# Performance work log

Measured on AMD Instinct MI355X. Metric: run time of the kernel, lower is better.

Reference implementation:

```python
import jax, jax.numpy as jnp
import numpy as np

N, T, S = 8192, 512, 32
D = 256          # d_model (h_states feature dim)
H = 256          # query_mlp_hidden_dim
R = 256          # operator rank
RFF = 64
DT = 16
L = 2            # num_query_mlp_layers
NHEAD = 4
HD = H // NHEAD
EPS = 1e-5


def _ln(x, g, b):
    m = jnp.mean(x, axis=-1, keepdims=True)
    v = jnp.mean((x - m) ** 2, axis=-1, keepdims=True)
    return (x - m) * jax.lax.rsqrt(v + EPS) * g + b


def _lin(x, w, b):  # torch Linear: w is [out, in]
    return x @ w.T + b


def rff_encode(x, B):
    p = x @ B
    return jnp.concatenate([jnp.cos(p), jnp.sin(p)], axis=-1)


def setup_inputs() -> dict:
    key = jax.random.key(0)
    ks = iter(jax.random.split(key, 64))
    rn = lambda shape, s=0.05: jax.random.normal(next(ks), shape, jnp.float32) * s
    inp = {}
    inp['xy'] = jax.random.uniform(next(ks), (N, 2), jnp.float32) * 2 * np.pi
    inp['t_q'] = jax.random.uniform(next(ks), (N,), jnp.float32)
    inp['c'] = jax.random.randint(next(ks), (N,), 0, 3)
    inp['h_states'] = rn((T, S, D), 1.0)
    inp['sensor_time'] = jnp.sort(jax.random.uniform(next(ks), (T,), jnp.float32))
    inp['B'] = rn((2, RFF), 1.0)
    q_in = 2 * RFF + DT + 8
    inp['time_w'] = rn((DT, 1)); inp['time_b'] = jnp.zeros((DT,))
    inp['comp_emb'] = rn((3, 8), 0.1)
    inp['trunk_in_w'] = rn((H, q_in)); inp['trunk_in_b'] = jnp.zeros((H,))
    inp['blk_ln_g'] = jnp.ones((L, H)); inp['blk_ln_b'] = jnp.zeros((L, H))
    inp['blk_fc1_w'] = rn((L, H, H)); inp['blk_fc1_b'] = jnp.zeros((L, H))
    inp['blk_fc2_w'] = rn((L, H, H)); inp['blk_fc2_b'] = jnp.zeros((L, H))
    inp['btp_w'] = rn((H, D)); inp['btp_b'] = jnp.zeros((H,))
    inp['bn_g'] = jnp.ones((H,)); inp['bn_b'] = jnp.zeros((H,))
    inp['attn_in_w'] = rn((3 * H, H)); inp['attn_in_b'] = jnp.zeros((3 * H,))
    inp['attn_out_w'] = rn((H, H)); inp['attn_out_b'] = jnp.zeros((H,))
    inp['bc_ln_g'] = jnp.ones((H,)); inp['bc_ln_b'] = jnp.zeros((H,))
    inp['bc_w1'] = rn((H, H)); inp['bc_b1'] = jnp.zeros((H,))
    inp['bc_w2'] = rn((H, H)); inp['bc_b2'] = jnp.zeros((H,))
    inp['trunk_out_w'] = rn((3 * R, H)); inp['trunk_out_b'] = jnp.zeros((3 * R,))
    inp['bproj_w'] = rn((3 * R, H)); inp['bproj_b'] = jnp.zeros((3 * R,))
    inp['log_temp'] = jnp.asarray(np.log(1.0 / np.sqrt(R)), jnp.float32)
    inp['comp_scale'] = jnp.ones((3,)); inp['comp_bias'] = jnp.zeros((3,))
    return inp


def reference(xy, t_q, c, h_states, sensor_time, B, time_w, time_b, comp_emb,
              trunk_in_w, trunk_in_b, blk_ln_g, blk_ln_b, blk_fc1_w, blk_fc1_b,
              blk_fc2_w, blk_fc2_b, btp_w, btp_b, bn_g, bn_b,
              attn_in_w, attn_in_b, attn_out_w, attn_out_b,
              bc_ln_g, bc_ln_b, bc_w1, bc_b1, bc_w2, bc_b2,
              trunk_out_w, trunk_out_b, bproj_w, bproj_b,
              log_temp, comp_scale, comp_bias):
    n = xy.shape[0]
    # time-indexed gather of CfC states
    idx = jnp.searchsorted(sensor_time, t_q, side='right') - 1
    idx = jnp.clip(idx, 0, h_states.shape[0] - 1)
    h_br = h_states[idx]                                   # [N,S,D]
    dt = jnp.maximum(t_q - sensor_time[idx], 0.0)          # [N]
    # trunk path
    rff = rff_encode(xy, B)                                # [N,2*RFF]
    time_e = _lin(dt[:, None], time_w, time_b)             # [N,DT]
    emb_c = comp_emb[c]                                    # [N,8]
    feat = jax.nn.silu(_lin(jnp.concatenate([rff, time_e, emb_c], -1), trunk_in_w, trunk_in_b))
    for i in range(blk_fc1_w.shape[0]):
        y = _ln(feat, blk_ln_g[i], blk_ln_b[i])
        y = jax.nn.silu(_lin(y, blk_fc1_w[i], blk_fc1_b[i]))
        feat = feat + _lin(y, blk_fc2_w[i], blk_fc2_b[i])
    trunk_basis = _lin(feat, trunk_out_w, trunk_out_b).reshape(n, 3, -1)
    # branch path: single-query cross attention over sensor tokens
    tokens = _lin(h_br, btp_w, btp_b)                      # [N,S,H]
    q_in = _ln(feat, bn_g, bn_b)                           # [N,H]
    wq, wk, wv = jnp.split(attn_in_w, 3, axis=0)
    bq, bk, bv = jnp.split(attn_in_b, 3, axis=0)
    q = (q_in @ wq.T + bq).reshape(n, NHEAD, HD)           # [N,h,d]
    k = (tokens @ wk.T + bk).reshape(n, S, NHEAD, HD)
    v = (tokens @ wv.T + bv).reshape(n, S, NHEAD, HD)
    scores = jnp.einsum('nhd,nshd->nhs', q, k) / jnp.sqrt(jnp.asarray(HD, q.dtype))
    attn = jax.nn.softmax(scores, axis=-1)
    ctx = jnp.einsum('nhs,nshd->nhd', attn, v).reshape(n, -1)
    ctx = ctx @ attn_out_w.T + attn_out_b                  # [N,H]
    y = _ln(ctx, bc_ln_g, bc_ln_b)
    y = jax.nn.silu(_lin(y, bc_w1, bc_b1))
    ctx = ctx + _lin(y, bc_w2, bc_b2)
    branch_basis = _lin(ctx, bproj_w, bproj_b).reshape(n, 3, -1)
    # per-component select + rank-contraction fusion
    ar = jnp.arange(n)
    trunk_sel = trunk_basis[ar, c]                         # [N,R]
    branch_sel = branch_basis[ar, c]
    temp = jnp.exp(log_temp).astype(trunk_sel.dtype)
    out = jnp.sum(trunk_sel * branch_sel, axis=1, keepdims=True) * temp
    return out * comp_scale[c][:, None] + comp_bias[c][:, None]
```

## Files before the change

kernel.cpp:

```cpp
#include <hip/hip_runtime.h>
#include <cstdint>
#include <cstddef>

typedef unsigned short u16;
typedef __attribute__((ext_vector_type(8))) short s16x8;
typedef __attribute__((ext_vector_type(4))) float f32x4;

#define NQ   8192
#define TT   512
#define STOK 32
#define LDF  260

__device__ __forceinline__ float b2f(u16 u) {
    return __uint_as_float(((uint32_t)u) << 16);
}
__device__ __forceinline__ u16 f2b(float f) {
    uint32_t x = __float_as_uint(f);
    uint32_t r = (x + 0x7FFFu + ((x >> 16) & 1u)) >> 16;
    return (u16)r;
}
__device__ __forceinline__ float silu_f(float x) { return x / (1.f + expf(-x)); }

__global__ __launch_bounds__(256) void const_kernel(float v, float* __restrict__ out) {
    int i = blockIdx.x * 256 + threadIdx.x;
    if (i < NQ) out[i] = v;
}

__global__ __launch_bounds__(256) void zero_kernel(int* __restrict__ cnt) {
    int i = blockIdx.x * 256 + threadIdx.x;
    if (i < 512) cnt[i] = 0;
}

__global__ __launch_bounds__(256) void feat32_kernel(
    const float* __restrict__ xy, const float* __restrict__ t_q,
    const int* __restrict__ c, const float* __restrict__ st,
    const float* __restrict__ B, const float* __restrict__ tw,
    const float* __restrict__ tb, const float* __restrict__ ce,
    float* __restrict__ FIN, int* __restrict__ IDX) {
    int n = blockIdx.x, t = threadIdx.x;
    float tq = t_q[n];
    int lo = 0, hi = TT;
    while (lo < hi) {
        int mid = (lo + hi) >> 1;
        if (st[mid] <= tq) lo = mid + 1; else hi = mid;
    }
    int idx = lo - 1;
    if (idx < 0) idx = 0;
    float dt = tq - st[idx];
    if (dt < 0.f) dt = 0.f;
    if (t == 0) IDX[n] = idx;
    float x = xy[2 * n], y = xy[2 * n + 1];
    size_t base = (size_t)n * 160;
    if (t < 64) { float p = x * B[t] + y * B[64 + t]; FIN[base + t] = cosf(p); }
    else if (t < 128) { int j = t - 64; float p = x * B[j] + y * B[64 + j]; FIN[base + t] = sinf(p); }
    else if (t < 144) { int j = t - 128; FIN[base + t] = dt * tw[j] + tb[j]; }
    else if (t < 152) { int j = t - 144; FIN[base + t] = ce[c[n] * 8 + j]; }
    else if (t < 160) { FIN[base + t] = 0.f; }
}

__global__ __launch_bounds__(256) void pack_split(
    const float* __restrict__ f1w, const float* __restrict__ f2w,
    const float* __restrict__ aiw, const float* __restrict__ aow,
    const float* __restrict__ w1, const float* __restrict__ w2,
    const float* __restrict__ tiw,
    u16* __restrict__ PH, u16* __restrict__ PL) {
    int i = blockIdx.x * 256 + threadIdx.x;
    if (i >= 565248) return;
    float v;
    size_t pos;
    if (i < 524288) {
        int m = i >> 16, j = i & 65535;
        int col = j >> 8, k = j & 255;
        const float* src;
        switch (m) {
            case 0: src = f1w; break;
            case 1: src = f1w + 65536; break;
            case 2: src = f2w; break;
            case 3: src = f2w + 65536; break;
            case 4: src = aiw; break;
            case 5: src = aow; break;
            case 6: src = w1; break;
            default: src = w2; break;
        }
        v = src[j];
        int ct = col >> 4, m16 = col & 15, k0 = k >> 5, quad = (k >> 3) & 3, jj = k & 7;
        pos = (size_t)m * 65536 + (size_t)(((ct * 8 + k0) * 64 + quad * 16 + m16) * 8 + jj);
    } else {
        int j = i - 524288;
        int col = j / 160, k = j % 160;
        v = (k < 152) ? tiw[col * 152 + k] : 0.f;
        int ct = col >> 4, m16 = col & 15, k0 = k >> 5, quad = (k >> 3) & 3, jj = k & 7;
        pos = 524288 + (size_t)(((ct * 5 + k0) * 64 + quad * 16 + m16) * 8 + jj);
    }
    u16 h = f2b(v);
    PH[pos] = h;
    PL[pos] = f2b(v - b2f(h));
}

__global__ __launch_bounds__(256) void combine_kv32(
    const float* __restrict__ aiw, const float* __restrict__ aib,
    const float* __restrict__ btw, const float* __restrict__ btb,
    u16* __restrict__ WKVb, float* __restrict__ bkv) {
    int kv = blockIdx.x >> 8, m = blockIdx.x & 255;
    int d = threadIdx.x;
    __shared__ float wrow[256];
    wrow[d] = aiw[(size_t)(kv + 1) * 65536 + (size_t)m * 256 + d];
    __syncthreads();
    float acc = 0.f;
#pragma unroll 8
    for (int o = 0; o < 256; o++) acc += wrow[o] * btw[(size_t)o * 256 + d];
    WKVb[(size_t)kv * 65536 + (size_t)m * 256 + d] = f2b(acc);
    float pb = wrow[d] * btb[d];
#pragma unroll
    for (int mm = 32; mm >= 1; mm >>= 1) pb += __shfl_xor(pb, mm);
    __shared__ float red[4];
    if ((d & 63) == 0) red[d >> 6] = pb;
    __syncthreads();
    if (d == 0)
        bkv[kv * 256 + m] = red[0] + red[1] + red[2] + red[3] + aib[(kv + 1) * 256 + m];
}

__global__ __launch_bounds__(256) void mcat_kernel(const float* __restrict__ tow,
                                                   const float* __restrict__ bpw,
                                                   u16* __restrict__ MCATb) {
    const int cc = blockIdx.z;
    const int t0 = blockIdx.x * 16, k0 = blockIdx.y * 16;
    const int lt = threadIdx.x & 15, lj = threadIdx.x >> 4;
    const int ot = threadIdx.x & 15, ok = threadIdx.x >> 4;
    __shared__ float As[16][17], Bs[16][17];
    float acc = 0.f;
    for (int j0 = 0; j0 < 256; j0 += 16) {
        As[lj][lt] = tow[((size_t)cc * 256 + j0 + lj) * 256 + t0 + lt];
        Bs[lj][lt] = bpw[((size_t)cc * 256 + j0 + lj) * 256 + k0 + lt];
        __syncthreads();
#pragma unroll
        for (int jj = 0; jj < 16; jj++) acc += As[jj][ot] * Bs[jj][ok];
        __syncthreads();
    }
    MCATb[((size_t)cc * 256 + t0 + ot) * 256 + k0 + ok] = f2b(acc);
}

__global__ __launch_bounds__(256) void uvs_kernel(
    const float* __restrict__ tow, const float* __restrict__ tob,
    const float* __restrict__ bpw, const float* __restrict__ bpb,
    float* __restrict__ U, float* __restrict__ V, float* __restrict__ S) {
    const int cc = blockIdx.x, t = threadIdx.x;
    float v = 0.f, u = 0.f;
    for (int r = 0; r < 256; r++) {
        v += tow[((size_t)cc * 256 + r) * 256 + t] * bpb[cc * 256 + r];
        u += bpw[((size_t)cc * 256 + r) * 256 + t] * tob[cc * 256 + r];
    }
    V[cc * 256 + t] = v;
    U[cc * 256 + t] = u;
    float sp = tob[cc * 256 + t] * bpb[cc * 256 + t];
#pragma unroll
    for (int m = 32; m >= 1; m >>= 1) sp += __shfl_xor(sp, m);
    __shared__ float red[4];
    if ((t & 63) == 0) red[t >> 6] = sp;
    __syncthreads();
    if (t == 0) S[cc] = red[0] + red[1] + red[2] + red[3];
}

__global__ __launch_bounds__(256) void hist_kernel(const int* __restrict__ IDX,
                                                   int* __restrict__ cnt) {
    int n = blockIdx.x * 256 + threadIdx.x;
    if (n < NQ) atomicAdd(&cnt[IDX[n]], 1);
}
__global__ __launch_bounds__(512) void scan_kernel(const int* __restrict__ cnt,
                                                   int* __restrict__ base,
                                                   int* __restrict__ cur) {
    __shared__ int s[TT];
    int t = threadIdx.x;
    int v = cnt[t];
    s[t] = v;
    __syncthreads();
    for (int off = 1; off < TT; off <<= 1) {
        int add = (t >= off) ? s[t - off] : 0;
        __syncthreads();
        s[t] += add;
        __syncthreads();
    }
    base[t] = s[t] - v;
    cur[t] = s[t] - v;
}
__global__ __launch_bounds__(256) void scat_kernel(const int* __restrict__ IDX,
                                                   int* __restrict__ cur,
                                                   int* __restrict__ perm) {
    int n = blockIdx.x * 256 + threadIdx.x;
    if (n < NQ) {
        int pos = atomicAdd(&cur[IDX[n]], 1);
        perm[pos] = n;
    }
}

template <int ST16, int SEL>
__global__ __launch_bounds__(256) void mgemm_b(
    const float* __restrict__ A, const u16* __restrict__ Wb,
    const float* __restrict__ bias, const int* __restrict__ csel,
    void* __restrict__ Cv, int ldc) {
    __shared__ u16 As[64 * 40];
    __shared__ u16 Ws[64 * 40];
    const int t = threadIdx.x;
    const size_t rb = (size_t)blockIdx.x * 64;
    const size_t cb = (size_t)blockIdx.y * 64;
    const int wave = t >> 6, lane = t & 63;
    const int m16 = lane & 15, quad = lane >> 4;
    const int sr = t >> 2, sk = (t & 3) * 8;
    const float* Ap = A + (rb + sr) * 256 + sk;
    const u16* Wp = Wb + (cb + sr) * 256 + sk;

    f32x4 acc[4] = {};
    for (int k0 = 0; k0 < 256; k0 += 32) {
        float4 a0 = *(const float4*)(Ap + k0);
        float4 a1 = *(const float4*)(Ap + k0 + 4);
        u16 ta[8] = {f2b(a0.x), f2b(a0.y), f2b(a0.z), f2b(a0.w),
                     f2b(a1.x), f2b(a1.y), f2b(a1.z), f2b(a1.w)};
        *(uint4*)&As[sr * 40 + sk] = *(const uint4*)ta;
        *(uint4*)&Ws[sr * 40 + sk] = *(const uint4*)(Wp + k0);
        __syncthreads();
        s16x8 af = *(const s16x8*)&As[(wave * 16 + m16) * 40 + quad * 8];
#pragma unroll
        for (int ct = 0; ct < 4; ct++) {
            s16x8 bf = *(const s16x8*)&Ws[(ct * 16 + m16) * 40 + quad * 8];
            acc[ct] = __builtin_amdgcn_mfma_f32_16x16x32_bf16(af, bf, acc[ct], 0, 0, 0);
        }
        __syncthreads();
    }
#pragma unroll
    for (int ct = 0; ct < 4; ct++) {
        size_t col = cb + ct * 16 + m16;
        float bb = bias ? bias[col] : 0.f;
#pragma unroll
        for (int r = 0; r < 4; r++) {
            size_t row = rb + wave * 16 + quad * 4 + r;
            float x = acc[ct][r] + bb;
            if (SEL) {
                int comp = (int)(col >> 8);
                if (csel[row] == comp)
                    ((float*)Cv)[row * 256 + (col & 255)] = x;
            } else if (ST16) {
                ((u16*)Cv)[row * (size_t)ldc + col] = f2b(x);
            } else {
                ((float*)Cv)[row * (size_t)ldc + col] = x;
            }
        }
    }
}

template <int NK0>
struct WF { s16x8 h[NK0], l[NK0]; };

template <int NK0>
__device__ __forceinline__ void wload(const u16* __restrict__ PH,
                                      const u16* __restrict__ PL, size_t mb,
                                      int wave, int lane, WF<NK0>& w) {
#pragma unroll
    for (int k0 = 0; k0 < NK0; k0++) {
        const size_t wo = mb + ((size_t)(wave * NK0 + k0) * 64 + lane) * 8;
        w.h[k0] = *(const s16x8*)&PH[wo];
        w.l[k0] = *(const s16x8*)&PL[wo];
    }
}

template <int NK0>
__device__ __forceinline__ void cgemm_c(const WF<NK0>& w,
                                        const u16* Ch, const u16* Cl,
                                        int lane, f32x4 (&acc)[2]) {
    acc[0] = (f32x4){0.f, 0.f, 0.f, 0.f};
    acc[1] = (f32x4){0.f, 0.f, 0.f, 0.f};
#pragma unroll
    for (int k0 = 0; k0 < NK0; k0++) {
        s16x8 a0h = *(const s16x8*)&Ch[(k0 * 64 + lane) * 8];
        s16x8 a0l = *(const s16x8*)&Cl[(k0 * 64 + lane) * 8];
        s16x8 a1h = *(const s16x8*)&Ch[((8 + k0) * 64 + lane) * 8];
        s16x8 a1l = *(const s16x8*)&Cl[((8 + k0) * 64 + lane) * 8];
        acc[0] = __builtin_amdgcn_mfma_f32_16x16x32_bf16(a0h, w.h[k0], acc[0], 0, 0, 0);
        acc[0] = __builtin_amdgcn_mfma_f32_16x16x32_bf16(a0l, w.h[k0], acc[0], 0, 0, 0);
        acc[0] = __builtin_amdgcn_mfma_f32_16x16x32_bf16(a0h, w.l[k0], acc[0], 0, 0, 0);
        acc[1] = __builtin_amdgcn_mfma_f32_16x16x32_bf16(a1h, w.h[k0], acc[1], 0, 0, 0);
        acc[1] = __builtin_amdgcn_mfma_f32_16x16x32_bf16(a1l, w.h[k0], acc[1], 0, 0, 0);
        acc[1] = __builtin_amdgcn_mfma_f32_16x16x32_bf16(a1h, w.l[k0], acc[1], 0, 0, 0);
    }
}

__device__ __forceinline__ void ln_split(const float* __restrict__ Fv,
                                         u16* __restrict__ Ch, u16* __restrict__ Cl,
                                         const float* __restrict__ g,
                                         const float* __restrict__ b,
                                         float* __restrict__ mean_s,
                                         float* __restrict__ rstd_s, int t) {
    {
        const int row = t >> 5, q = t & 31;
        const float* fr = Fv + row * LDF;
        float4 v0 = *(const float4*)&fr[q * 4];
        float4 v1 = *(const float4*)&fr[q * 4 + 128];
        float s1 = v0.x + v0.y + v0.z + v0.w + v1.x + v1.y + v1.z + v1.w;
        float s2 = v0.x * v0.x + v0.y * v0.y + v0.z * v0.z + v0.w * v0.w +
                   v1.x * v1.x + v1.y * v1.y + v1.z * v1.z + v1.w * v1.w;
#pragma unroll
        for (int m = 16; m >= 1; m >>= 1) {
            s1 += __shfl_xor(s1, m);
            s2 += __shfl_xor(s2, m);
        }
        if (q == 0) {
            float mean = s1 * (1.f / 256.f);
            mean_s[row] = mean;
            rstd_s[row] = rsqrtf(s2 * (1.f / 256.f) - mean * mean + 1e-5f);
        }
    }
    __syncthreads();
    {
        const int rw = t & 31, qc = t >> 5;
        const float* fr = Fv + rw * LDF + qc * 8;
        float4 v0 = *(const float4*)fr;
        float4 v1 = *(const float4*)(fr + 4);
        const float mean = mean_s[rw], rstd = rstd_s[rw];
        float4 g0 = *(const float4*)&g[qc * 8], g1 = *(const float4*)&g[qc * 8 + 4];
        float4 b0 = *(const float4*)&b[qc * 8], b1 = *(const float4*)&b[qc * 8 + 4];
        float va[8] = {v0.x, v0.y, v0.z, v0.w, v1.x, v1.y, v1.z, v1.w};
        float ga[8] = {g0.x, g0.y, g0.z, g0.w, g1.x, g1.y, g1.z, g1.w};
        float ba[8] = {b0.x, b0.y, b0.z, b0.w, b1.x, b1.y, b1.z, b1.w};
        u16 hv[8], lv[8];
#pragma unroll
        for (int j = 0; j < 8; j++) {
            float x = (va[j] - mean) * rstd * ga[j] + ba[j];
            hv[j] = f2b(x);
            lv[j] = f2b(x - b2f(hv[j]));
        }
        const int c = qc * 8;
        const int off = (((rw >> 4) * 8 + (c >> 5)) * 64 +
                         (((c >> 3) & 3) * 16 + (rw & 15))) * 8;
        *(uint4*)&Ch[off] = *(const uint4*)hv;
        *(uint4*)&Cl[off] = *(const uint4*)lv;
    }
}

__global__ __launch_bounds__(1024) void chain1_kernel(
    const float* __restrict__ FIN, const u16* __restrict__ PH,
    const u16* __restrict__ PL, const float* __restrict__ tib,
    const float* __restrict__ lng, const float* __restrict__ lnb,
    const float* __restrict__ f1b, const float* __restrict__ f2bv,
    const float* __restrict__ bng, const float* __restrict__ bnb,
    const float* __restrict__ aib,
    float* __restrict__ Qb, float* __restrict__ Fg) {
    __shared__ u16 Ch[8192], Cl[8192];
    __shared__ float Fv[32 * LDF];
    __shared__ float mean_s[32], rstd_s[32];
    const int t = threadIdx.x;
    const int wave = t >> 6, lane = t & 63;
    const int m16 = lane & 15, quad = lane >> 4;
    const size_t rb = (size_t)blockIdx.x * 32;
    const int col = wave * 16 + m16;
    f32x4 acc[2];

    {
        const int row = t >> 5, q = t & 31;
        if (q < 20) {
            const float* p = FIN + (rb + row) * 160 + q * 8;
            float4 v0 = *(const float4*)p, v1 = *(const float4*)(p + 4);
            float va[8] = {v0.x, v0.y, v0.z, v0.w, v1.x, v1.y, v1.z, v1.w};
            u16 hv[8], lv[8];
#pragma unroll
            for (int j = 0; j < 8; j++) { hv[j] = f2b(va[j]); lv[j] = f2b(va[j] - b2f(hv[j])); }
            const int c = q * 8;
            const int off = (((row >> 4) * 8 + (c >> 5)) * 64 +
                             (((c >> 3) & 3) * 16 + (row & 15))) * 8;
            *(uint4*)&Ch[off] = *(const uint4*)hv;
            *(uint4*)&Cl[off] = *(const uint4*)lv;
        }
    }

    {
        WF<5> w;
        wload<5>(PH, PL, 524288, wave, lane, w);
        __syncthreads();
        cgemm_c<5>(w, Ch, Cl, lane, acc);
    }
    {
        const float bb = tib[col];
#pragma unroll
        for (int rt = 0; rt < 2; rt++)
#pragma unroll
            for (int r = 0; r < 4; r++)
                Fv[(rt * 16 + quad * 4 + r) * LDF + col] = silu_f(acc[rt][r] + bb);
    }
    __syncthreads();

#pragma unroll
    for (int L = 0; L < 2; L++) {
        ln_split(Fv, Ch, Cl, lng + L * 256, lnb + L * 256, mean_s, rstd_s, t);
        {
            WF<8> w;
            wload<8>(PH, PL, (size_t)L * 65536, wave, lane, w);
            __syncthreads();
            cgemm_c<8>(w, Ch, Cl, lane, acc);
        }
        __syncthreads();
        {
            const float bb = f1b[L * 256 + col];
            const int k0c = col >> 5, qc4 = (col >> 3) & 3, jc = col & 7;
#pragma unroll
            for (int rt = 0; rt < 2; rt++)
#pragma unroll
                for (int r = 0; r < 4; r++) {
                    const int row = rt * 16 + quad * 4 + r;
                    float x = silu_f(acc[rt][r] + bb);
                    const int off = ((rt * 8 + k0c) * 64 + (qc4 * 16 + (row & 15))) * 8 + jc;
                    u16 h = f2b(x);
                    Ch[off] = h;
                    Cl[off] = f2b(x - b2f(h));
                }
        }
        {
            WF<8> w;
            wload<8>(PH, PL, 131072 + (size_t)L * 65536, wave, lane, w);
            __syncthreads();
            cgemm_c<8>(w, Ch, Cl, lane, acc);
        }
        {
            const float bb = f2bv[L * 256 + col];
#pragma unroll
            for (int rt = 0; rt < 2; rt++)
#pragma unroll
                for (int r = 0; r < 4; r++) {
                    const int row = rt * 16 + quad * 4 + r;
                    Fv[row * LDF + col] += acc[rt][r] + bb;
                }
        }
        __syncthreads();
    }

    {
        const int row = t >> 5, q = t & 31;
        const float* fr = Fv + row * LDF + q * 8;
        float4 v0 = *(const float4*)fr, v1 = *(const float4*)(fr + 4);
        float* dst = Fg + (rb + row) * 256 + q * 8;
        *(float4*)dst = v0;
        *(float4*)(dst + 4) = v1;
    }
    ln_split(Fv, Ch, Cl, bng, bnb, mean_s, rstd_s, t);

    {
        WF<8> w;
        wload<8>(PH, PL, 262144, wave, lane, w);
        __syncthreads();
        cgemm_c<8>(w, Ch, Cl, lane, acc);
    }
    {
        const float bb = aib[col];
#pragma unroll
        for (int rt = 0; rt < 2; rt++)
#pragma unroll
            for (int r = 0; r < 4; r++) {
                const int row = rt * 16 + quad * 4 + r;
                Qb[(rb + row) * 256 + col] = acc[rt][r] + bb;
            }
    }
}

__global__ __launch_bounds__(1024) void chain2_kernel(
    const float* __restrict__ CTX, const u16* __restrict__ PH,
    const u16* __restrict__ PL, const float* __restrict__ aob,
    const float* __restrict__ clg, const float* __restrict__ clb,
    const float* __restrict__ b1, const float* __restrict__ b2v,
    float* __restrict__ C2g) {
    __shared__ u16 Ch[8192], Cl[8192];
    __shared__ float Fv[32 * LDF];
    __shared__ float mean_s[32], rstd_s[32];
    const int t = threadIdx.x;
    const int wave = t >> 6, lane = t & 63;
    const int m16 = lane & 15, quad = lane >> 4;
    const size_t rb = (size_t)blockIdx.x * 32;
    const int col = wave * 16 + m16;
    f32x4 acc[2];

    {
        const int row = t >> 5, q = t & 31;
        const float* p = CTX + (rb + row) * 256 + q * 8;
        float4 v0 = *(const float4*)p, v1 = *(const float4*)(p + 4);
        float va[8] = {v0.x, v0.y, v0.z, v0.w, v1.x, v1.y, v1.z, v1.w};
        u16 hv[8], lv[8];
#pragma unroll
        for (int j = 0; j < 8; j++) { hv[j] = f2b(va[j]); lv[j] = f2b(va[j] - b2f(hv[j])); }
        const int c = q * 8;
        const int off = (((row >> 4) * 8 + (c >> 5)) * 64 +
                         (((c >> 3) & 3) * 16 + (row & 15))) * 8;
        *(uint4*)&Ch[off] = *(const uint4*)hv;
        *(uint4*)&Cl[off] = *(const uint4*)lv;
    }

    {
        WF<8> w;
        wload<8>(PH, PL, 327680, wave, lane, w);
        __syncthreads();
        cgemm_c<8>(w, Ch, Cl, lane, acc);
    }
    {
        const float bb = aob[col];
#pragma unroll
        for (int rt = 0; rt < 2; rt++)
#pragma unroll
            for (int r = 0; r < 4; r++)
                Fv[(rt * 16 + quad * 4 + r) * LDF + col] = acc[rt][r] + bb;
    }
    __syncthreads();

    ln_split(Fv, Ch, Cl, clg, clb, mean_s, rstd_s, t);
    {
        WF<8> w;
        wload<8>(PH, PL, 393216, wave, lane, w);
        __syncthreads();
        cgemm_c<8>(w, Ch, Cl, lane, acc);
    }
    __syncthreads();
    {
        const float bb = b1[col];
        const int k0c = col >> 5, qc4 = (col >> 3) & 3, jc = col & 7;
#pragma unroll
        for (int rt = 0; rt < 2; rt++)
#pragma unroll
            for (int r = 0; r < 4; r++) {
                const int row = rt * 16 + quad * 4 + r;
                float x = silu_f(acc[rt][r] + bb);
                const int off = ((rt * 8 + k0c) * 64 + (qc4 * 16 + (row & 15))) * 8 + jc;
                u16 h = f2b(x);
                Ch[off] = h;
                Cl[off] = f2b(x - b2f(h));
            }
    }
    {
        WF<8> w;
        wload<8>(PH, PL, 458752, wave, lane, w);
        __syncthreads();
        cgemm_c<8>(w, Ch, Cl, lane, acc);
    }
    {
        const float bb = b2v[col];
#pragma unroll
        for (int rt = 0; rt < 2; rt++)
#pragma unroll
            for (int r = 0; r < 4; r++) {
                const int row = rt * 16 + quad * 4 + r;
                C2g[(rb + row) * 256 + col] = acc[rt][r] + bb + Fv[row * LDF + col];
            }
    }
}

__global__ __launch_bounds__(256) void attn4_kernel(
    float* __restrict__ QC, const u16* __restrict__ KV,
    const int* __restrict__ idx, const int* __restrict__ perm) {
    __shared__ u16 vsh[STOK * 264];
    __shared__ float qsh[256], attw[4][STOK];
    const int n = perm[blockIdx.x];
    const int t = threadIdx.x;
    qsh[t] = QC[(size_t)n * 256 + t];
    int ii = idx[n];
    ii = ii < 0 ? 0 : (ii > TT - 1 ? TT - 1 : ii);
    const u16* kvb = KV + (size_t)ii * STOK * 512;
#pragma unroll
    for (int i = t; i < 1024; i += 256) {
        int s = i >> 5, dq = (i & 31) * 8;
        *(uint4*)&vsh[s * 264 + dq] = *(const uint4*)&kvb[(size_t)s * 512 + 256 + dq];
    }
    __syncthreads();
    if (t < 128) {
        int h = t >> 5, s = t & 31;
        const u16* kp = kvb + (size_t)s * 512 + h * 64;
        uint4 kv[8];
#pragma unroll
        for (int dq = 0; dq < 8; dq++) kv[dq] = *(const uint4*)(kp + dq * 8);
        float p0 = 0.f, p1 = 0.f;
#pragma unroll
        for (int dq = 0; dq < 8; dq++) {
            const u16* ks = (const u16*)&kv[dq];
            float a0 = 0.f;
#pragma unroll
            for (int j = 0; j < 8; j++) a0 += qsh[h * 64 + dq * 8 + j] * b2f(ks[j]);
            if (dq & 1) p1 += a0; else p0 += a0;
        }
        float sc = (p0 + p1) * 0.125f;
        float mx = sc;
#pragma unroll
        for (int m = 16; m >= 1; m >>= 1) mx = fmaxf(mx, __shfl_xor(mx, m));
        float e = expf(sc - mx);
        float sum = e;
#pragma unroll
        for (int m = 16; m >= 1; m >>= 1) sum += __shfl_xor(sum, m);
        attw[h][s] = e / sum;
    }
    __syncthreads();
    {
        int h = t >> 6;
        float a = 0.f;
#pragma unroll 8
        for (int s = 0; s < STOK; s++) a += attw[h][s] * b2f(vsh[s * 264 + t]);
        QC[(size_t)n * 256 + t] = a;
    }
}

__global__ __launch_bounds__(256) void dot_kernel(
    const float* __restrict__ F, const float* __restrict__ H,
    const float* __restrict__ C2, const int* __restrict__ c,
    const float* __restrict__ U, const float* __restrict__ V,
    const float* __restrict__ S, const float* __restrict__ lt,
    const float* __restrict__ cs, const float* __restrict__ cbv,
    float* __restrict__ out) {
    const int n = blockIdx.x * 4 + (threadIdx.x >> 6);
    const int lane = threadIdx.x & 63;
    const int cc = c[n];
    float4 f4 = *(const float4*)&F[(size_t)n * 256 + lane * 4];
    float4 h4 = *(const float4*)&H[(size_t)n * 256 + lane * 4];
    float4 g4 = *(const float4*)&C2[(size_t)n * 256 + lane * 4];
    float4 v4 = *(const float4*)&V[cc * 256 + lane * 4];
    float4 u4 = *(const float4*)&U[cc * 256 + lane * 4];
    float a = f4.x * (h4.x + v4.x) + f4.y * (h4.y + v4.y) +
              f4.z * (h4.z + v4.z) + f4.w * (h4.w + v4.w) +
              u4.x * g4.x + u4.y * g4.y + u4.z * g4.z + u4.w * g4.w;
#pragma unroll
    for (int m = 32; m >= 1; m >>= 1) a += __shfl_xor(a, m);
    if (lane == 0)
        out[n] = (a + S[cc]) * expf(lt[0]) * cs[cc] + cbv[cc];
}

extern "C" void kernel_launch(void* const* d_in, const int* in_sizes, int n_in,
                              void* d_out, int out_size, void* d_ws, size_t ws_size,
                              hipStream_t stream) {
    float* out = (float*)d_out;
    const dim3 blk(256);

    static const int EXPECT[38] = {
        16384, 8192, 8192, 4194304, 512, 128, 16, 16, 24,
        38912, 256, 512, 512, 131072, 512, 131072, 512,
        65536, 256, 256, 256, 196608, 768, 65536, 256,
        256, 256, 65536, 256, 65536, 256, 196608, 768,
        196608, 768, 1, 3, 3};
    if (n_in != 38) { const_kernel<<<NQ / 256, blk, 0, stream>>>(99.0e6f, out); return; }
    for (int i = 0; i < 38; i++)
        if (in_sizes[i] != EXPECT[i]) {
            const_kernel<<<NQ / 256, blk, 0, stream>>>((100.0f + i) * 1.0e6f, out);
            return;
        }

    const float* xy  = (const float*)d_in[0];
    const float* tq  = (const float*)d_in[1];
    const int*   c   = (const int*)d_in[2];
    const float* hs  = (const float*)d_in[3];
    const float* st  = (const float*)d_in[4];
    const float* Bm  = (const float*)d_in[5];
    const float* tw  = (const float*)d_in[6];
    const float* tbv = (const float*)d_in[7];
    const float* ce  = (const float*)d_in[8];
    const float* tiw = (const float*)d_in[9];
    const float* tib = (const float*)d_in[10];
    const float* lng = (const float*)d_in[11];
    const float* lnb = (const float*)d_in[12];
    const float* f1w = (const float*)d_in[13];
    const float* f1b = (const float*)d_in[14];
    const float* f2w = (const float*)d_in[15];
    const float* f2b_ = (const float*)d_in[16];
    const float* btw = (const float*)d_in[17];
    const float* btb = (const float*)d_in[18];
    const float* bng = (const float*)d_in[19];
    const float* bnb = (const float*)d_in[20];
    const float* aiw = (const float*)d_in[21];
    const float* aib = (const float*)d_in[22];
    const float* aow = (const float*)d_in[23];
    const float* aob = (const float*)d_in[24];
    const float* clg = (const float*)d_in[25];
    const float* clb = (const float*)d_in[26];
    const float* w1  = (const float*)d_in[27];
    const float* b1  = (const float*)d_in[28];
    const float* w2  = (const float*)d_in[29];
    const float* b2  = (const float*)d_in[30];
    const float* tow = (const float*)d_in[31];
    const float* tob = (const float*)d_in[32];
    const float* bpw = (const float*)d_in[33];
    const float* bpb = (const float*)d_in[34];
    const float* lt  = (const float*)d_in[35];
    const float* cs  = (const float*)d_in[36];
    const float* cbv = (const float*)d_in[37];

    char* ws = (char*)d_ws;
    const size_t MB = 1 << 20;
    if (ws_size < 44 * MB) {
        const_kernel<<<NQ / 256, blk, 0, stream>>>(8.0e6f, out);
        return;
    }

    u16*   KV   = (u16*)(ws + 0 * MB);
    char*  S_A  = ws + 16 * MB;
    char*  S_B  = ws + 24 * MB;
    char*  S_C  = ws + 32 * MB;
    char*  misc = ws + 40 * MB;
    float* FIN  = (float*)S_A;
    float* H    = (float*)S_A;
    float* F    = (float*)S_B;
    float* Qb   = (float*)S_C;
    float* C2   = (float*)S_C;
    int*   IDX  = (int*)(misc + 0);
    float* bkv  = (float*)(misc + 32 * 1024);
    float* Ubuf = (float*)(misc + 36 * 1024);
    float* Vbuf = (float*)(misc + 40 * 1024);
    float* Sbuf = (float*)(misc + 44 * 1024);
    int*   CNT  = (int*)(misc + 48 * 1024);
    int*   BASE = (int*)(misc + 52 * 1024);
    int*   CUR  = (int*)(misc + 56 * 1024);
    int*   PERM = (int*)(misc + 60 * 1024);
    u16*   WKVb = (u16*)(misc + 92 * 1024);
    u16*   MCATb= (u16*)(misc + 348 * 1024);
    u16*   PH   = (u16*)(misc + 732 * 1024);
    u16*   PL   = (u16*)(misc + 1836 * 1024);

    const dim3 gKV(TT * STOK / 64, 8);
    const dim3 gSEL(NQ / 64, 12);

    zero_kernel<<<2, blk, 0, stream>>>(CNT);
    pack_split<<<2208, blk, 0, stream>>>(f1w, f2w, aiw, aow, w1, w2, tiw, PH, PL);
    combine_kv32<<<512, blk, 0, stream>>>(aiw, aib, btw, btb, WKVb, bkv);
    mcat_kernel<<<dim3(16, 16, 3), blk, 0, stream>>>(tow, bpw, MCATb);
    uvs_kernel<<<3, blk, 0, stream>>>(tow, tob, bpw, bpb, Ubuf, Vbuf, Sbuf);
    feat32_kernel<<<NQ, blk, 0, stream>>>(xy, tq, c, st, Bm, tw, tbv, ce, FIN, IDX);

    hist_kernel<<<NQ / 256, blk, 0, stream>>>(IDX, CNT);
    scan_kernel<<<1, dim3(512), 0, stream>>>(CNT, BASE, CUR);
    scat_kernel<<<NQ / 256, blk, 0, stream>>>(IDX, CUR, PERM);

    mgemm_b<1, 0><<<gKV, blk, 0, stream>>>(hs, WKVb, bkv, nullptr, KV, 512);

    chain1_kernel<<<NQ / 32, dim3(1024), 0, stream>>>(FIN, PH, PL, tib, lng, lnb,
                                                      f1b, f2b_, bng, bnb, aib, Qb, F);
    attn4_kernel<<<NQ, blk, 0, stream>>>(Qb, KV, IDX, PERM);
    chain2_kernel<<<NQ / 32, dim3(1024), 0, stream>>>(Qb, PH, PL, aob, clg, clb,
                                                      b1, b2, C2);
    mgemm_b<0, 1><<<gSEL, blk, 0, stream>>>(C2, MCATb, nullptr, c, H, 256);
    dot_kernel<<<NQ / 4, blk, 0, stream>>>(F, H, C2, c, Ubuf, Vbuf, Sbuf, lt, cs, cbv, out);
}
```

Measured before the change: 322.1 us.

## Fuse weight-prep and feature kernels into one block-dispatched launch

Merges pack_split, combine_kv32, mcat_kernel, uvs_kernel and feat32_kernel into a single prep_all kernel that picks its role by block index ranges. The uvs work is also split from 3 blocks into 24 blocks that combine partial sums with atomicAdd, and zero_kernel now zeroes U and V first. The aim is to remove several launch gaps and the serial tail of the long 3-block uvs kernel. In exchange, all roles share one register/LDS footprint, and float atomics make the order of the U/V summation nondeterministic.

Measured after the change: 286.2 us. 11.2% less time.

```diff
diff --git a/kernel.cpp b/kernel.cpp
--- a/kernel.cpp
+++ b/kernel.cpp
@@ -11,6 +11,12 @@
 #define STOK 32
 #define LDF  260
 
+#define PB_PACK 2208
+#define PB_COMB (PB_PACK + 512)
+#define PB_MCAT (PB_COMB + 768)
+#define PB_UVS  (PB_MCAT + 24)
+#define PB_TOT  (PB_UVS + NQ)
+
 __device__ __forceinline__ float b2f(u16 u) {
     return __uint_as_float(((uint32_t)u) << 16);
 }
@@ -26,139 +32,144 @@
     if (i < NQ) out[i] = v;
 }
 
-__global__ __launch_bounds__(256) void zero_kernel(int* __restrict__ cnt) {
+__global__ __launch_bounds__(256) void zero_kernel(int* __restrict__ cnt,
+                                                   float* __restrict__ U,
+                                                   float* __restrict__ V) {
     int i = blockIdx.x * 256 + threadIdx.x;
     if (i < 512) cnt[i] = 0;
-}
-
-__global__ __launch_bounds__(256) void feat32_kernel(
+    else if (i < 1280) U[i - 512] = 0.f;
+    else if (i < 2048) V[i - 1280] = 0.f;
+}
+
+__global__ __launch_bounds__(256) void prep_all(
+    const float* __restrict__ f1w, const float* __restrict__ f2w,
+    const float* __restrict__ aiw, const float* __restrict__ aow,
+    const float* __restrict__ w1, const float* __restrict__ w2,
+    const float* __restrict__ tiw,
+    u16* __restrict__ PH, u16* __restrict__ PL,
+    const float* __restrict__ aib, const float* __restrict__ btw,
+    const float* __restrict__ btb, u16* __restrict__ WKVb,
+    float* __restrict__ bkv,
+    const float* __restrict__ tow, const float* __restrict__ bpw,
+    u16* __restrict__ MCATb,
+    const float* __restrict__ tob, const float* __restrict__ bpb,
+    float* __restrict__ U, float* __restrict__ V, float* __restrict__ S,
     const float* __restrict__ xy, const float* __restrict__ t_q,
     const int* __restrict__ c, const float* __restrict__ st,
     const float* __restrict__ B, const float* __restrict__ tw,
     const float* __restrict__ tb, const float* __restrict__ ce,
     float* __restrict__ FIN, int* __restrict__ IDX) {
-    int n = blockIdx.x, t = threadIdx.x;
-    float tq = t_q[n];
-    int lo = 0, hi = TT;
-    while (lo < hi) {
-        int mid = (lo + hi) >> 1;
-        if (st[mid] <= tq) lo = mid + 1; else hi = mid;
-    }
-    int idx = lo - 1;
-    if (idx < 0) idx = 0;
-    float dt = tq - st[idx];
-    if (dt < 0.f) dt = 0.f;
-    if (t == 0) IDX[n] = idx;
-    float x = xy[2 * n], y = xy[2 * n + 1];
-    size_t base = (size_t)n * 160;
-    if (t < 64) { float p = x * B[t] + y * B[64 + t]; FIN[base + t] = cosf(p); }
-    else if (t < 128) { int j = t - 64; float p = x * B[j] + y * B[64 + j]; FIN[base + t] = sinf(p); }
-    else if (t < 144) { int j = t - 128; FIN[base + t] = dt * tw[j] + tb[j]; }
-    else if (t < 152) { int j = t - 144; FIN[base + t] = ce[c[n] * 8 + j]; }
-    else if (t < 160) { FIN[base + t] = 0.f; }
-}
-
-__global__ __launch_bounds__(256) void pack_split(
-    const float* __restrict__ f1w, const float* __restrict__ f2w,
-    const float* __restrict__ aiw, const float* __restrict__ aow,
-    const float* __restrict__ w1, const float* __restrict__ w2,
-    const float* __restrict__ tiw,
-    u16* __restrict__ PH, u16* __restrict__ PL) {
-    int i = blockIdx.x * 256 + threadIdx.x;
-    if (i >= 565248) return;
-    float v;
-    size_t pos;
-    if (i < 524288) {
-        int m = i >> 16, j = i & 65535;
-        int col = j >> 8, k = j & 255;
-        const float* src;
-        switch (m) {
-            case 0: src = f1w; break;
-            case 1: src = f1w + 65536; break;
-            case 2: src = f2w; break;
-            case 3: src = f2w + 65536; break;
-            case 4: src = aiw; break;
-            case 5: src = aow; break;
-            case 6: src = w1; break;
-            default: src = w2; break;
-        }
-        v = src[j];
-        int ct = col >> 4, m16 = col & 15, k0 = k >> 5, quad = (k >> 3) & 3, jj = k & 7;
-        pos = (size_t)m * 65536 + (size_t)(((ct * 8 + k0) * 64 + quad * 16 + m16) * 8 + jj);
+    __shared__ float As2[16][17], Bs2[16][17];
+    __shared__ float wrow[256];
+    __shared__ float red[4];
+    const int b = blockIdx.x;
+    const int t = threadIdx.x;
+
+    if (b < PB_PACK) {
+        int i = b * 256 + t;
+        if (i >= 565248) return;
+        float v;
+        size_t pos;
+        if (i < 524288) {
+            int m = i >> 16, j = i & 65535;
+            int col = j >> 8, k = j & 255;
+            const float* src;
+            switch (m) {
+                case 0: src = f1w; break;
+                case 1: src = f1w + 65536; break;
+                case 2: src = f2w; break;
+                case 3: src = f2w + 65536; break;
+                case 4: src = aiw; break;
+                case 5: src = aow; break;
+                case 6: src = w1; break;
+                default: src = w2; break;
+            }
+            v = src[j];
+            int ct = col >> 4, m16 = col & 15, k0 = k >> 5, quad = (k >> 3) & 3, jj = k & 7;
+            pos = (size_t)m * 65536 + (size_t)(((ct * 8 + k0) * 64 + quad * 16 + m16) * 8 + jj);
+        } else {
+            int j = i - 524288;
+            int col = j / 160, k = j % 160;
+            v = (k < 152) ? tiw[col * 152 + k] : 0.f;
+            int ct = col >> 4, m16 = col & 15, k0 = k >> 5, quad = (k >> 3) & 3, jj = k & 7;
+            pos = 524288 + (size_t)(((ct * 5 + k0) * 64 + quad * 16 + m16) * 8 + jj);
+        }
+        u16 h = f2b(v);
+        PH[pos] = h;
+        PL[pos] = f2b(v - b2f(h));
+    } else if (b < PB_COMB) {
+        int bb = b - PB_PACK;
+        int kv = bb >> 8, m = bb & 255;
+        int d = t;
+        wrow[d] = aiw[(size_t)(kv + 1) * 65536 + (size_t)m * 256 + d];
+        __syncthreads();
+        float acc = 0.f;
+#pragma unroll 8
+        for (int o = 0; o < 256; o++) acc += wrow[o] * btw[(size_t)o * 256 + d];
+        WKVb[(size_t)kv * 65536 + (size_t)m * 256 + d] = f2b(acc);
+        float pb = wrow[d] * btb[d];
+#pragma unroll
+        for (int mm = 32; mm >= 1; mm >>= 1) pb += __shfl_xor(pb, mm);
+        if ((d & 63) == 0) red[d >> 6] = pb;
+        __syncthreads();
+        if (d == 0)
+            bkv[kv * 256 + m] = red[0] + red[1] + red[2] + red[3] + aib[(kv + 1) * 256 + m];
+    } else if (b < PB_MCAT) {
+        int m = b - PB_COMB;
+        const int cc = m >> 8;
+        const int rem = m & 255;
+        const int t0 = (rem >> 4) * 16, k0 = (rem & 15) * 16;
+        const int lt = t & 15, lj = t >> 4;
+        const int ot = t & 15, ok = t >> 4;
+        float acc = 0.f;
+        for (int j0 = 0; j0 < 256; j0 += 16) {
+            As2[lj][lt] = tow[((size_t)cc * 256 + j0 + lj) * 256 + t0 + lt];
+            Bs2[lj][lt] = bpw[((size_t)cc * 256 + j0 + lj) * 256 + k0 + lt];
+            __syncthreads();
+#pragma unroll
+            for (int jj = 0; jj < 16; jj++) acc += As2[jj][ot] * Bs2[jj][ok];
+            __syncthreads();
+        }
+        MCATb[((size_t)cc * 256 + t0 + ot) * 256 + k0 + ok] = f2b(acc);
+    } else if (b < PB_UVS) {
+        int m = b - PB_MCAT;
+        const int cc = m / 8, j = m % 8;
+        float v = 0.f, u = 0.f;
+        for (int r = j * 32; r < j * 32 + 32; r++) {
+            v += tow[((size_t)cc * 256 + r) * 256 + t] * bpb[cc * 256 + r];
+            u += bpw[((size_t)cc * 256 + r) * 256 + t] * tob[cc * 256 + r];
+        }
+        atomicAdd(&V[cc * 256 + t], v);
+        atomicAdd(&U[cc * 256 + t], u);
+        if (j == 0) {
+            float sp = tob[cc * 256 + t] * bpb[cc * 256 + t];
+#pragma unroll
+            for (int mm = 32; mm >= 1; mm >>= 1) sp += __shfl_xor(sp, mm);
+            if ((t & 63) == 0) red[t >> 6] = sp;
+            __syncthreads();
+            if (t == 0) S[cc] = red[0] + red[1] + red[2] + red[3];
+        }
     } else {
-        int j = i - 524288;
-        int col = j / 160, k = j % 160;
-        v = (k < 152) ? tiw[col * 152 + k] : 0.f;
-        int ct = col >> 4, m16 = col & 15, k0 = k >> 5, quad = (k >> 3) & 3, jj = k & 7;
-        pos = 524288 + (size_t)(((ct * 5 + k0) * 64 + quad * 16 + m16) * 8 + jj);
-    }
-    u16 h = f2b(v);
-    PH[pos] = h;
-    PL[pos] = f2b(v - b2f(h));
-}
-
-__global__ __launch_bounds__(256) void combine_kv32(
-    const float* __restrict__ aiw, const float* __restrict__ aib,
-    const float* __restrict__ btw, const float* __restrict__ btb,
-    u16* __restrict__ WKVb, float* __restrict__ bkv) {
-    int kv = blockIdx.x >> 8, m = blockIdx.x & 255;
-    int d = threadIdx.x;
-    __shared__ float wrow[256];
-    wrow[d] = aiw[(size_t)(kv + 1) * 65536 + (size_t)m * 256 + d];
-    __syncthreads();
-    float acc = 0.f;
-#pragma unroll 8
-    for (int o = 0; o < 256; o++) acc += wrow[o] * btw[(size_t)o * 256 + d];
-    WKVb[(size_t)kv * 65536 + (size_t)m * 256 + d] = f2b(acc);
-    float pb = wrow[d] * btb[d];
-#pragma unroll
-    for (int mm = 32; mm >= 1; mm >>= 1) pb += __shfl_xor(pb, mm);
-    __shared__ float red[4];
-    if ((d & 63) == 0) red[d >> 6] = pb;
-    __syncthreads();
-    if (d == 0)
-        bkv[kv * 256 + m] = red[0] + red[1] + red[2] + red[3] + aib[(kv + 1) * 256 + m];
-}
-
-__global__ __launch_bounds__(256) void mcat_kernel(const float* __restrict__ tow,
-                                                   const float* __restrict__ bpw,
-                                                   u16* __restrict__ MCATb) {
-    const int cc = blockIdx.z;
-    const int t0 = blockIdx.x * 16, k0 = blockIdx.y * 16;
-    const int lt = threadIdx.x & 15, lj = threadIdx.x >> 4;
-    const int ot = threadIdx.x & 15, ok = threadIdx.x >> 4;
-    __shared__ float As[16][17], Bs[16][17];
-    float acc = 0.f;
-    for (int j0 = 0; j0 < 256; j0 += 16) {
-        As[lj][lt] = tow[((size_t)cc * 256 + j0 + lj) * 256 + t0 + lt];
-        Bs[lj][lt] = bpw[((size_t)cc * 256 + j0 + lj) * 256 + k0 + lt];
-        __syncthreads();
-#pragma unroll
-        for (int jj = 0; jj < 16; jj++) acc += As[jj][ot] * Bs[jj][ok];
-        __syncthreads();
-    }
-    MCATb[((size_t)cc * 256 + t0 + ot) * 256 + k0 + ok] = f2b(acc);
-}
-
-__global__ __launch_bounds__(256) void uvs_kernel(
-    const float* __restrict__ tow, const float* __restrict__ tob,
-    const float* __restrict__ bpw, const float* __restrict__ bpb,
-    float* __restrict__ U, float* __restrict__ V, float* __restrict__ S) {
-    const int cc = blockIdx.x, t = threadIdx.x;
-    float v = 0.f, u = 0.f;
-    for (int r = 0; r < 256; r++) {
-        v += tow[((size_t)cc * 256 + r) * 256 + t] * bpb[cc * 256 + r];
-        u += bpw[((size_t)cc * 256 + r) * 256 + t] * tob[cc * 256 + r];
-    }
-    V[cc * 256 + t] = v;
-    U[cc * 256 + t] = u;
-    float sp = tob[cc * 256 + t] * bpb[cc * 256 + t];
-#pragma unroll
-    for (int m = 32; m >= 1; m >>= 1) sp += __shfl_xor(sp, m);
-    __shared__ float red[4];
-    if ((t & 63) == 0) red[t >> 6] = sp;
-    __syncthreads();
-    if (t == 0) S[cc] = red[0] + red[1] + red[2] + red[3];
+        int n = b - PB_UVS;
+        float tq = t_q[n];
+        int lo = 0, hi = TT;
+        while (lo < hi) {
+            int mid = (lo + hi) >> 1;
+            if (st[mid] <= tq) lo = mid + 1; else hi = mid;
+        }
+        int idx = lo - 1;
+        if (idx < 0) idx = 0;
+        float dt = tq - st[idx];
+        if (dt < 0.f) dt = 0.f;
+        if (t == 0) IDX[n] = idx;
+        float x = xy[2 * n], y = xy[2 * n + 1];
+        size_t base = (size_t)n * 160;
+        if (t < 64) { float p = x * B[t] + y * B[64 + t]; FIN[base + t] = cosf(p); }
+        else if (t < 128) { int j = t - 64; float p = x * B[j] + y * B[64 + j]; FIN[base + t] = sinf(p); }
+        else if (t < 144) { int j = t - 128; FIN[base + t] = dt * tw[j] + tb[j]; }
+        else if (t < 152) { int j = t - 144; FIN[base + t] = ce[c[n] * 8 + j]; }
+        else if (t < 160) { FIN[base + t] = 0.f; }
+    }
 }
 
 __global__ __launch_bounds__(256) void hist_kernel(const int* __restrict__ IDX,
@@ -714,12 +725,13 @@
     const dim3 gKV(TT * STOK / 64, 8);
     const dim3 gSEL(NQ / 64, 12);
 
-    zero_kernel<<<2, blk, 0, stream>>>(CNT);
-    pack_split<<<2208, blk, 0, stream>>>(f1w, f2w, aiw, aow, w1, w2, tiw, PH, PL);
-    combine_kv32<<<512, blk, 0, stream>>>(aiw, aib, btw, btb, WKVb, bkv);
-    mcat_kernel<<<dim3(16, 16, 3), blk, 0, stream>>>(tow, bpw, MCATb);
-    uvs_kernel<<<3, blk, 0, stream>>>(tow, tob, bpw, bpb, Ubuf, Vbuf, Sbuf);
-    feat32_kernel<<<NQ, blk, 0, stream>>>(xy, tq, c, st, Bm, tw, tbv, ce, FIN, IDX);
+    zero_kernel<<<8, blk, 0, stream>>>(CNT, Ubuf, Vbuf);
+    prep_all<<<PB_TOT, blk, 0, stream>>>(
+        f1w, f2w, aiw, aow, w1, w2, tiw, PH, PL,
+        aib, btw, btb, WKVb, bkv,
+        tow, bpw, MCATb,
+        tob, bpb, Ubuf, Vbuf, Sbuf,
+        xy, tq, c, st, Bm, tw, tbv, ce, FIN, IDX);
 
     hist_kernel<<<NQ / 256, blk, 0, stream>>>(IDX, CNT);
     scan_kernel<<<1, dim3(512), 0, stream>>>(CNT, BASE, CUR);
```
